# Optimization experiments

Measured on AMD Instinct MI355X. Metric: run time of the kernel, lower is better.

## Reference

```python
import jax, jax.numpy as jnp
import numpy as np

N = 20000
K = 13          # kernel_size**3 // 2 for kernel_size=3
INP = 32
OUT = 32


def setup_inputs() -> dict:
    key = jax.random.key(0)
    k1, k2, k3, k4, k5, k6 = jax.random.split(key, 6)
    feats = jax.random.normal(k1, (N, INP), dtype=jnp.float32)
    coords = jax.random.uniform(k2, (N, 3), dtype=jnp.float32)
    W = jax.random.normal(k3, (3, INP * OUT), dtype=jnp.float32) * 0.1
    b = jax.random.normal(k4, (INP * OUT,), dtype=jnp.float32) * 0.01
    nbr_idx = jax.random.randint(k5, (N, K), 0, N, dtype=jnp.int32)
    nbr_mask = jax.random.randint(k6, (N, K), 0, 2, dtype=jnp.int32).astype(bool)
    return {"feats": feats, "coords": coords, "W": W, "b": b,
            "nbr_idx": nbr_idx, "nbr_mask": nbr_mask}


def reference(feats, coords, W, b, nbr_idx, nbr_mask):
    # Gather neighbor features / xyz per kernel offset; missing pairs stay 0
    # (matches torch scatter into zero-initialized neis / rel_xyz tensors).
    m = nbr_mask[..., None]                      # [N, K, 1]
    neis = jnp.where(m, feats[nbr_idx], 0.0)     # [N, K, INP]
    rel_xyz = jnp.where(m, coords[nbr_idx], 0.0)  # [N, K, 3]
    # Tiny linear generates per-(point, offset) weight tensors.
    weights = (rel_xyz @ W + b).reshape(N, K, INP, OUT)  # [N, K, INP, OUT]
    # Weighted sum reduce over kernel offsets and input channels.
    out = jnp.einsum('nkio,nki->no', weights, neis)      # [N, OUT]
    return out
```

## Files before the change

kernel.cpp:

```cpp
#include <hip/hip_runtime.h>
#include <hip/hip_bf16.h>

#define NPTS 20000
#define KNB 13
#define CH 32
#define PPW 4
#define WVB 4
#define PTS_PER_BLOCK (PPW * WVB)
#define NBLOCKS (NPTS / PTS_PER_BLOCK)

typedef __attribute__((ext_vector_type(8))) short bf16x8;
typedef __attribute__((ext_vector_type(4))) float f32x4;

static __device__ __forceinline__ short f2bf(float x) {
    union { float f; unsigned u; } v; v.f = x;
    return (short)((v.u + 0x8000u) >> 16);
}

__global__ __launch_bounds__(256) void fused_conv(
    const float* __restrict__ feats, const float* __restrict__ coords,
    const float* __restrict__ W, const float* __restrict__ bias,
    const int* __restrict__ nbr_idx, const unsigned char* __restrict__ mask_b,
    float* __restrict__ out) {

    const int l   = threadIdx.x & 63;
    const int w   = threadIdx.x >> 6;
    const int r15 = l & 15;
    const int g   = l >> 4;
    const int k8  = g * 8;

    const int p0 = l * 4;
    const int pred = (mask_b[p0 + 1] | mask_b[p0 + 2] | mask_b[p0 + 3]) != 0;
    const bool bytes_mode = (__ballot(pred) != 0ull);

    bf16x8 bF[4][2];
    #pragma unroll
    for (int kt = 0; kt < 4; ++kt) {
        const float* src = (kt < 3) ? (W + kt * (CH * CH)) : bias;
        #pragma unroll
        for (int nt = 0; nt < 2; ++nt) {
            #pragma unroll
            for (int e = 0; e < 8; ++e)
                bF[kt][nt][e] = f2bf(src[(k8 + e) * CH + nt * 16 + r15]);
        }
    }

    const int n0 = (blockIdx.x * WVB + w) * PPW;

    #pragma unroll
    for (int pp = 0; pp < PPW; ++pp) {
        const int n = n0 + pp;

        int valid = 0, j = 0;
        if (r15 < KNB) {
            const int p = n * KNB + r15;
            j = nbr_idx[p];
            const int mv = bytes_mode ? (int)mask_b[p] : ((const int*)mask_b)[p];
            valid = (mv != 0);
        }
        const int ja = valid ? j : 0;

        const float4* fp = (const float4*)(feats + ja * CH + k8);
        const float4 fa = fp[0], fb = fp[1];
        const float f[8] = {fa.x, fa.y, fa.z, fa.w, fb.x, fb.y, fb.z, fb.w};
        const float vs = valid ? 1.0f : 0.0f;
        const float c0 = coords[ja * 3 + 0] * vs;
        const float c1 = coords[ja * 3 + 1] * vs;
        const float c2 = coords[ja * 3 + 2] * vs;

        bf16x8 a0, a1, a2, a3;
        #pragma unroll
        for (int e = 0; e < 8; ++e) {
            const float fe = f[e];
            a0[e] = f2bf(fe * c0);
            a1[e] = f2bf(fe * c1);
            a2[e] = f2bf(fe * c2);
            a3[e] = f2bf(fe * vs);
        }

        f32x4 acc0 = {0.f, 0.f, 0.f, 0.f};
        f32x4 acc1 = {0.f, 0.f, 0.f, 0.f};
        acc0 = __builtin_amdgcn_mfma_f32_16x16x32_bf16(a0, bF[0][0], acc0, 0, 0, 0);
        acc1 = __builtin_amdgcn_mfma_f32_16x16x32_bf16(a0, bF[0][1], acc1, 0, 0, 0);
        acc0 = __builtin_amdgcn_mfma_f32_16x16x32_bf16(a1, bF[1][0], acc0, 0, 0, 0);
        acc1 = __builtin_amdgcn_mfma_f32_16x16x32_bf16(a1, bF[1][1], acc1, 0, 0, 0);
        acc0 = __builtin_amdgcn_mfma_f32_16x16x32_bf16(a2, bF[2][0], acc0, 0, 0, 0);
        acc1 = __builtin_amdgcn_mfma_f32_16x16x32_bf16(a2, bF[2][1], acc1, 0, 0, 0);
        acc0 = __builtin_amdgcn_mfma_f32_16x16x32_bf16(a3, bF[3][0], acc0, 0, 0, 0);
        acc1 = __builtin_amdgcn_mfma_f32_16x16x32_bf16(a3, bF[3][1], acc1, 0, 0, 0);

        float s0 = acc0[0] + acc0[1] + acc0[2] + acc0[3];
        float s1 = acc1[0] + acc1[1] + acc1[2] + acc1[3];
        s0 += __shfl_xor(s0, 16); s0 += __shfl_xor(s0, 32);
        s1 += __shfl_xor(s1, 16); s1 += __shfl_xor(s1, 32);

        if (l < 32) out[n * CH + l] = (l < 16) ? s0 : s1;
    }
}

extern "C" void kernel_launch(void* const* d_in, const int* in_sizes, int n_in,
                              void* d_out, int out_size, void* d_ws, size_t ws_size,
                              hipStream_t stream) {
    const float* feats  = (const float*)d_in[0];
    const float* coords = (const float*)d_in[1];
    const float* W      = (const float*)d_in[2];
    const float* bias   = (const float*)d_in[3];
    const int*   nidx   = (const int*)d_in[4];
    const unsigned char* nmask = (const unsigned char*)d_in[5];
    float* out = (float*)d_out;

    fused_conv<<<NBLOCKS, 256, 0, stream>>>(feats, coords, W, bias, nidx, nmask, out);
}
```

Before: 14.33 us.

## Factor coordinate scaling out of MFMA inputs and apply after matmul

Each neighbor's A fragment becomes the plain feature vector instead of four coordinate-scaled copies. The per-neighbor coordinate weights are applied afterwards to the eight independent MFMA outputs through lane shuffles, which removes the multiply-and-convert work for three extra operand sets. The eight MFMAs no longer chain on shared accumulators, so they can issue back to back, but this adds 16 shuffles, more accumulator registers and an FMA reduction per point. Neighbor index loads are also made unconditional by clamping the lane index, which removes a branch.

```diff
diff --git a/kernel.cpp b/kernel.cpp
--- a/kernel.cpp
+++ b/kernel.cpp
@@ -33,16 +33,14 @@
     const int pred = (mask_b[p0 + 1] | mask_b[p0 + 2] | mask_b[p0 + 3]) != 0;
     const bool bytes_mode = (__ballot(pred) != 0ull);
 
-    bf16x8 bF[4][2];
+    bf16x8 bF[8];
     #pragma unroll
-    for (int kt = 0; kt < 4; ++kt) {
-        const float* src = (kt < 3) ? (W + kt * (CH * CH)) : bias;
+    for (int q = 0; q < 8; ++q) {
+        const float* src = (q < 6) ? (W + (q >> 1) * (CH * CH)) : bias;
+        const int ocol = (q & 1) * 16 + r15;
         #pragma unroll
-        for (int nt = 0; nt < 2; ++nt) {
-            #pragma unroll
-            for (int e = 0; e < 8; ++e)
-                bF[kt][nt][e] = f2bf(src[(k8 + e) * CH + nt * 16 + r15]);
-        }
+        for (int e = 0; e < 8; ++e)
+            bF[q][e] = f2bf(src[(k8 + e) * CH + ocol]);
     }
 
     const int n0 = (blockIdx.x * WVB + w) * PPW;
@@ -51,46 +49,42 @@
     for (int pp = 0; pp < PPW; ++pp) {
         const int n = n0 + pp;
 
-        int valid = 0, j = 0;
-        if (r15 < KNB) {
-            const int p = n * KNB + r15;
-            j = nbr_idx[p];
-            const int mv = bytes_mode ? (int)mask_b[p] : ((const int*)mask_b)[p];
-            valid = (mv != 0);
-        }
+        const int rcl = (r15 < KNB) ? r15 : (KNB - 1);
+        const int p = n * KNB + rcl;
+        const int j = nbr_idx[p];
+        const int mv = bytes_mode ? (int)mask_b[p] : ((const int*)mask_b)[p];
+        const bool valid = (mv != 0) & (r15 < KNB);
         const int ja = valid ? j : 0;
+        const float vsv = valid ? 1.0f : 0.0f;
+        const float c0v = coords[ja * 3 + 0] * vsv;
+        const float c1v = coords[ja * 3 + 1] * vsv;
+        const float c2v = coords[ja * 3 + 2] * vsv;
 
         const float4* fp = (const float4*)(feats + ja * CH + k8);
         const float4 fa = fp[0], fb = fp[1];
         const float f[8] = {fa.x, fa.y, fa.z, fa.w, fb.x, fb.y, fb.z, fb.w};
-        const float vs = valid ? 1.0f : 0.0f;
-        const float c0 = coords[ja * 3 + 0] * vs;
-        const float c1 = coords[ja * 3 + 1] * vs;
-        const float c2 = coords[ja * 3 + 2] * vs;
+        bf16x8 aF;
+        #pragma unroll
+        for (int e = 0; e < 8; ++e) aF[e] = f2bf(f[e]);
 
-        bf16x8 a0, a1, a2, a3;
+        f32x4 acc[8];
         #pragma unroll
-        for (int e = 0; e < 8; ++e) {
-            const float fe = f[e];
-            a0[e] = f2bf(fe * c0);
-            a1[e] = f2bf(fe * c1);
-            a2[e] = f2bf(fe * c2);
-            a3[e] = f2bf(fe * vs);
+        for (int q = 0; q < 8; ++q) {
+            f32x4 z = {0.f, 0.f, 0.f, 0.f};
+            acc[q] = __builtin_amdgcn_mfma_f32_16x16x32_bf16(aF, bF[q], z, 0, 0, 0);
         }
 
-        f32x4 acc0 = {0.f, 0.f, 0.f, 0.f};
-        f32x4 acc1 = {0.f, 0.f, 0.f, 0.f};
-        acc0 = __builtin_amdgcn_mfma_f32_16x16x32_bf16(a0, bF[0][0], acc0, 0, 0, 0);
-        acc1 = __builtin_amdgcn_mfma_f32_16x16x32_bf16(a0, bF[0][1], acc1, 0, 0, 0);
-        acc0 = __builtin_amdgcn_mfma_f32_16x16x32_bf16(a1, bF[1][0], acc0, 0, 0, 0);
-        acc1 = __builtin_amdgcn_mfma_f32_16x16x32_bf16(a1, bF[1][1], acc1, 0, 0, 0);
-        acc0 = __builtin_amdgcn_mfma_f32_16x16x32_bf16(a2, bF[2][0], acc0, 0, 0, 0);
-        acc1 = __builtin_amdgcn_mfma_f32_16x16x32_bf16(a2, bF[2][1], acc1, 0, 0, 0);
-        acc0 = __builtin_amdgcn_mfma_f32_16x16x32_bf16(a3, bF[3][0], acc0, 0, 0, 0);
-        acc1 = __builtin_amdgcn_mfma_f32_16x16x32_bf16(a3, bF[3][1], acc1, 0, 0, 0);
-
-        float s0 = acc0[0] + acc0[1] + acc0[2] + acc0[3];
-        float s1 = acc1[0] + acc1[1] + acc1[2] + acc1[3];
+        float s0 = 0.f, s1 = 0.f;
+        #pragma unroll
+        for (int r = 0; r < 4; ++r) {
+            const int m = g * 4 + r;
+            const float w0 = __shfl(c0v, m);
+            const float w1 = __shfl(c1v, m);
+            const float w2 = __shfl(c2v, m);
+            const float w3 = __shfl(vsv, m);
+            s0 += w0 * acc[0][r] + w1 * acc[2][r] + w2 * acc[4][r] + w3 * acc[6][r];
+            s1 += w0 * acc[1][r] + w1 * acc[3][r] + w2 * acc[5][r] + w3 * acc[7][r];
+        }
         s0 += __shfl_xor(s0, 16); s0 += __shfl_xor(s0, 32);
         s1 += __shfl_xor(s1, 16); s1 += __shfl_xor(s1, 32);
 
```

Result: slower. 16.19 us (+13.0%).
